# Kernel optimization log

Measured on AMD Instinct MI355X. Metric: run time of the kernel, lower is better.

Reference implementation:

```python
import jax, jax.numpy as jnp
import numpy as np

N_HEADS = 2

def setup_inputs() -> dict:
    key = jax.random.key(0)
    ks = jax.random.split(key, 10)
    d, bank, b, t = 192, 1000, 16, 4096
    s = 1.0 / np.sqrt(d)
    return {
        "z": jax.random.normal(ks[0], (b, d, t), jnp.float32),
        "memory_bank": jax.random.normal(ks[1], (d, bank), jnp.float32),
        "Wq": jax.random.normal(ks[2], (d, d), jnp.float32) * s,
        "bq": jax.random.normal(ks[3], (d,), jnp.float32) * 0.02,
        "Wk": jax.random.normal(ks[4], (d, d), jnp.float32) * s,
        "bk": jax.random.normal(ks[5], (d,), jnp.float32) * 0.02,
        "Wv": jax.random.normal(ks[6], (d, d), jnp.float32) * s,
        "bv": jax.random.normal(ks[7], (d,), jnp.float32) * 0.02,
        "Wo": jax.random.normal(ks[8], (d, d), jnp.float32) * s,
        "bo": jax.random.normal(ks[9], (d,), jnp.float32) * 0.02,
    }


def _split_heads(x):
    # x: [b, d, t] -> [b, h, t, dk]  (matches view(b, h, dk, t).transpose(2, 3))
    b, d, t = x.shape
    dk = d // N_HEADS
    return x.reshape(b, N_HEADS, dk, t).transpose(0, 1, 3, 2)


def reference(z, memory_bank, Wq, bq, Wk, bk, Wv, bv, Wo, bo):
    b, d, t = z.shape
    dk = d // N_HEADS
    # memory bank expanded over batch: [b, d, bank]
    c = jnp.broadcast_to(memory_bank[None], (b,) + memory_bank.shape)
    # 1x1 conv projections == per-channel linear
    q = jnp.einsum('oc,bct->bot', Wq, z) + bq[None, :, None]
    k = jnp.einsum('oc,bcs->bos', Wk, c) + bk[None, :, None]
    v = jnp.einsum('oc,bcs->bos', Wv, c) + bv[None, :, None]
    qh = _split_heads(q)  # [b, h, t, dk]
    kh = _split_heads(k)  # [b, h, bank, dk]
    vh = _split_heads(v)  # [b, h, bank, dk]
    scores = jnp.einsum('bhtd,bhsd->bhts', qh, kh) / jnp.sqrt(jnp.asarray(dk, z.dtype))
    p = jax.nn.softmax(scores, axis=-1)  # [b, h, t, bank]
    out = jnp.einsum('bhts,bhsd->bhtd', p, vh)  # [b, h, t, dk]
    out = out.transpose(0, 1, 3, 2).reshape(b, d, t)  # merge heads -> [b, d, t]
    return jnp.einsum('oc,bct->bot', Wo, out) + bo[None, :, None]
```

## Files before the change

### kernel.cpp

```cpp
#include <hip/hip_runtime.h>


typedef float  f32x4  __attribute__((ext_vector_type(4)));
typedef __bf16 bf16;
typedef __bf16 bf16x8 __attribute__((ext_vector_type(8)));

#define B_   16
#define D_   192
#define T_   4096
#define BANK 1000
#define SP   1024
#define DK   96
#define SCALE 0.10206207261596577f
#define LOG2E 1.4426950408889634f

__global__ __launch_bounds__(256) void pre_kernel(
    const float* __restrict__ z, bf16* __restrict__ zT,
    const float* __restrict__ mb,
    const float* __restrict__ Wk, const float* __restrict__ bk,
    const float* __restrict__ Wv, const float* __restrict__ bv,
    bf16* __restrict__ ktg, bf16* __restrict__ vtg) {
  __shared__ __align__(16) bf16 sT[64 * 200];
  const int tid = threadIdx.x;
  if (blockIdx.y < 16) {
    const int t0 = blockIdx.x * 64, b = blockIdx.y;
#pragma unroll
    for (int it = 0; it < 48; ++it) {
      int e = tid + 256 * it;
      int c = e >> 6, tl = e & 63;
      sT[tl * 200 + c] = (bf16)z[((size_t)b * D_ + c) * T_ + t0 + tl];
    }
    __syncthreads();
#pragma unroll
    for (int it = 0; it < 6; ++it) {
      int g = tid + 256 * it;
      int tl = g / 24, c8 = (g % 24) * 8;
      bf16x8 v = *(const bf16x8*)&sT[tl * 200 + c8];
      *(bf16x8*)&zT[((size_t)b * T_ + t0 + tl) * D_ + c8] = v;
    }
  } else {
    int idx = (blockIdx.y - 16) * 64 + blockIdx.x;
    int s = (idx & 3) * 256 + tid;
    int o = idx >> 2;
    int h = o / DK, i = o % DK;
    float ak = 0.f, av = 0.f;
    if (s < BANK) {
      ak = bk[o]; av = bv[o];
      for (int c = 0; c < D_; ++c) {
        float m = mb[c * BANK + s];
        ak += Wk[o * D_ + c] * m;
        av += Wv[o * D_ + c] * m;
      }
    }
    ktg[(size_t)(h * SP + s) * DK + i] = (bf16)ak;
    vtg[(size_t)(h * DK + i) * SP + s] = (bf16)av;
  }
}

template <typename OT>
__global__ __launch_bounds__(256) void proj_kernel(
    const bf16* __restrict__ XT, const float* __restrict__ W,
    const float* __restrict__ bias, OT* __restrict__ Y, float outscale) {
  __shared__ __align__(16) char smem[40960];
  bf16* sA = (bf16*)smem;
  bf16* sB = (bf16*)(smem + 16384);
  float* sE = (float*)smem;

  const int tid = threadIdx.x;
  const int t0 = blockIdx.x * 256, o0 = blockIdx.y * 64, b = blockIdx.z;
  const int lane = tid & 63, wv = tid >> 6;
  const int quad = lane >> 4, l15 = lane & 15;

  const bf16* ap[4];
#pragma unroll
  for (int r = 0; r < 4; ++r) {
    int g = tid + 256 * r;
    int tg = g >> 6, qd = (g >> 4) & 3, l5 = g & 15;
    ap[r] = &XT[((size_t)b * T_ + t0 + tg * 16 + l5) * D_ + qd * 8];
  }
  bf16x8 areg[4];
#pragma unroll
  for (int r = 0; r < 4; ++r) areg[r] = *(const bf16x8*)ap[r];

#pragma unroll
  for (int r = 0; r < 6; ++r) {
    int g = tid + 256 * r;
    int kb = g >> 8, nt = (g >> 6) & 3, qd = (g >> 4) & 3, l5 = g & 15;
    const float* wp = &W[(o0 + nt * 16 + l5) * D_ + kb * 32 + qd * 8];
    f32x4 wa = *(const f32x4*)wp, wb = *(const f32x4*)(wp + 4);
    bf16x8 pk;
#pragma unroll
    for (int u = 0; u < 4; ++u) { pk[u] = (bf16)wa[u]; pk[4 + u] = (bf16)wb[u]; }
    *(bf16x8*)&sB[(size_t)g * 8] = pk;
  }

  f32x4 acc[4][4];
#pragma unroll
  for (int m = 0; m < 4; ++m)
#pragma unroll
    for (int n = 0; n < 4; ++n) acc[m][n] = (f32x4){0.f, 0.f, 0.f, 0.f};

  for (int kb = 0; kb < 6; ++kb) {
    __syncthreads();
#pragma unroll
    for (int r = 0; r < 4; ++r)
      *(bf16x8*)&sA[(size_t)(tid + 256 * r) * 8] = areg[r];
    __syncthreads();
    if (kb < 5) {
#pragma unroll
      for (int r = 0; r < 4; ++r)
        areg[r] = *(const bf16x8*)(ap[r] + (kb + 1) * 32);
    }
    bf16x8 bf[4];
#pragma unroll
    for (int n = 0; n < 4; ++n)
      bf[n] = *(const bf16x8*)&sB[(size_t)((kb * 4 + n) * 64 + lane) * 8];
#pragma unroll
    for (int m = 0; m < 4; ++m) {
      bf16x8 af = *(const bf16x8*)&sA[(size_t)((wv * 4 + m) * 64 + lane) * 8];
#pragma unroll
      for (int n = 0; n < 4; ++n)
        acc[m][n] = __builtin_amdgcn_mfma_f32_16x16x32_bf16(af, bf[n], acc[m][n], 0, 0, 0);
    }
  }
  __syncthreads();

  float bs[4];
#pragma unroll
  for (int n = 0; n < 4; ++n) bs[n] = bias[o0 + n * 16 + l15];
  float* se = sE + wv * 1088;
#pragma unroll
  for (int m = 0; m < 4; ++m) {
#pragma unroll
    for (int n = 0; n < 4; ++n)
#pragma unroll
      for (int r = 0; r < 4; ++r)
        se[(quad * 4 + r) * 68 + n * 16 + l15] = (acc[m][n][r] + bs[n]) * outscale;
#pragma unroll
    for (int oo = 0; oo < 16; ++oo) {
      int ol = oo * 4 + quad;
      Y[((size_t)b * D_ + o0 + ol) * T_ + t0 + wv * 64 + m * 16 + l15] =
          (OT)se[l15 * 68 + ol];
    }
  }
}

__global__ __launch_bounds__(512) void attn_kernel(
    const bf16* __restrict__ qws, const bf16* __restrict__ ktg,
    const bf16* __restrict__ vtg, bf16* __restrict__ owsT) {
  __shared__ __align__(16) char smem[32768];
  bf16* kt = (bf16*)smem;
  bf16* vt = (bf16*)(smem + 12288);
  bf16* sP = (bf16*)(smem + 24576);
  bf16* qt = (bf16*)smem;

  const int tid = threadIdx.x;
  const int t0 = blockIdx.x * 128, h = blockIdx.y, b = blockIdx.z;
  const int lane = tid & 63, wv = tid >> 6;
  const int quad = lane >> 4, l15 = lane & 15;

  const bf16* kb_g = ktg + (size_t)h * SP * DK;
  const bf16* vb_g = vtg + (size_t)h * DK * SP;

  const bf16* sp_ptr[3];
  int sp_str[3];
#pragma unroll
  for (int r = 0; r < 3; ++r) {
    int g = tid + 512 * r;
    if (g < 768) {
      int kb = g >> 8, n = (g >> 6) & 3, qd = (g >> 4) & 3, l5 = g & 15;
      sp_ptr[r] = kb_g + (size_t)(n * 16 + l5) * DK + kb * 32 + qd * 8;
      sp_str[r] = 64 * DK;
    } else {
      int gv = g - 768, blk = gv >> 6;
      int kbv = blk / 6, n = blk % 6, qd = (gv >> 4) & 3, l5 = gv & 15;
      sp_ptr[r] = vb_g + (size_t)(n * 16 + l5) * SP + kbv * 32 + qd * 8;
      sp_str[r] = 64;
    }
  }
  bf16x8 kreg[3];
#pragma unroll
  for (int r = 0; r < 3; ++r) kreg[r] = *(const bf16x8*)sp_ptr[r];

#pragma unroll
  for (int r = 0; r < 3; ++r) {
    int g8 = tid + 512 * r;
    int i = g8 >> 4, t8 = (g8 & 15) * 8;
    bf16x8 v = *(const bf16x8*)&qws[((size_t)(b * D_ + h * DK + i)) * T_ + t0 + t8];
    int kb = i >> 5, qd = (i >> 3) & 3, j = i & 7;
#pragma unroll
    for (int tt = 0; tt < 8; ++tt) {
      int t = t8 + tt;
      int G = (kb * 8 + (t >> 4)) * 64 + qd * 16 + (t & 15);
      int Gs = G ^ ((G >> 6) & 7);
      qt[(size_t)Gs * 8 + j] = v[tt];
    }
  }
  __syncthreads();
  bf16x8 qf[3];
#pragma unroll
  for (int kb = 0; kb < 3; ++kb) {
    int G = (kb * 8 + wv) * 64 + lane;
    int Gs = G ^ ((G >> 6) & 7);
    qf[kb] = *(const bf16x8*)&qt[(size_t)Gs * 8];
  }

  f32x4 oacc[6];
#pragma unroll
  for (int n = 0; n < 6; ++n) oacc[n] = (f32x4){0.f, 0.f, 0.f, 0.f};
  float m_run[4] = {-1e30f, -1e30f, -1e30f, -1e30f};
  float l_run[4] = {0.f, 0.f, 0.f, 0.f};

  for (int ch = 0; ch < 16; ++ch) {
    __syncthreads();
#pragma unroll
    for (int r = 0; r < 3; ++r)
      *(bf16x8*)(smem + (size_t)(tid + 512 * r) * 16) = kreg[r];
    __syncthreads();
    if (ch < 15) {
#pragma unroll
      for (int r = 0; r < 3; ++r) {
        sp_ptr[r] += sp_str[r];
        kreg[r] = *(const bf16x8*)sp_ptr[r];
      }
    }

    f32x4 sacc[4];
#pragma unroll
    for (int n = 0; n < 4; ++n) sacc[n] = (f32x4){0.f, 0.f, 0.f, 0.f};
#pragma unroll
    for (int kb = 0; kb < 3; ++kb) {
#pragma unroll
      for (int n = 0; n < 4; ++n) {
        bf16x8 bfm = *(const bf16x8*)&kt[(size_t)((kb * 4 + n) * 64 + lane) * 8];
        sacc[n] = __builtin_amdgcn_mfma_f32_16x16x32_bf16(qf[kb], bfm, sacc[n], 0, 0, 0);
      }
    }
    if (ch == 15) {
#pragma unroll
      for (int r = 0; r < 4; ++r) {
        if (l15 >= 8) sacc[2][r] = -1e30f;
        sacc[3][r] = -1e30f;
      }
    }

    float mc[4];
#pragma unroll
    for (int r = 0; r < 4; ++r) {
      float m0 = fmaxf(fmaxf(sacc[0][r], sacc[1][r]), fmaxf(sacc[2][r], sacc[3][r]));
      m0 = fmaxf(m0, __shfl_xor(m0, 1, 64));
      m0 = fmaxf(m0, __shfl_xor(m0, 2, 64));
      m0 = fmaxf(m0, __shfl_xor(m0, 4, 64));
      m0 = fmaxf(m0, __shfl_xor(m0, 8, 64));
      mc[r] = m0;
    }
    bool keep = (mc[0] - m_run[0] <= 8.f) && (mc[1] - m_run[1] <= 8.f) &&
                (mc[2] - m_run[2] <= 8.f) && (mc[3] - m_run[3] <= 8.f);
    if (!__all(keep)) {
#pragma unroll
      for (int r = 0; r < 4; ++r) {
        float mn = fmaxf(m_run[r], mc[r]);
        float al = exp2f(m_run[r] - mn);
        m_run[r] = mn;
        l_run[r] *= al;
#pragma unroll
        for (int n = 0; n < 6; ++n) oacc[n][r] *= al;
      }
    }
    float pr[4][4];
#pragma unroll
    for (int r = 0; r < 4; ++r) {
      float ls = 0.f;
#pragma unroll
      for (int n = 0; n < 4; ++n) { pr[n][r] = exp2f(sacc[n][r] - m_run[r]); ls += pr[n][r]; }
      ls += __shfl_xor(ls, 1, 64);
      ls += __shfl_xor(ls, 2, 64);
      ls += __shfl_xor(ls, 4, 64);
      ls += __shfl_xor(ls, 8, 64);
      l_run[r] += ls;
    }

#pragma unroll
    for (int kb = 0; kb < 2; ++kb) {
#pragma unroll
      for (int nn = 0; nn < 2; ++nn) {
        int n = kb * 2 + nn;
        int qd2 = (nn << 1) | (l15 >> 3), j = l15 & 7;
#pragma unroll
        for (int r = 0; r < 4; ++r) {
          int g0 = qd2 * 16 + quad * 4 + r;
          int gs = g0 ^ ((g0 >> 3) & 7);
          sP[(size_t)(wv * 64 + gs) * 8 + j] = (bf16)pr[n][r];
        }
      }
      int gl = lane ^ ((lane >> 3) & 7);
      bf16x8 pa = *(const bf16x8*)&sP[(size_t)(wv * 64 + gl) * 8];
#pragma unroll
      for (int n2 = 0; n2 < 6; ++n2) {
        bf16x8 vf = *(const bf16x8*)&vt[(size_t)((kb * 6 + n2) * 64 + lane) * 8];
        oacc[n2] = __builtin_amdgcn_mfma_f32_16x16x32_bf16(pa, vf, oacc[n2], 0, 0, 0);
      }
    }
  }

  float inv[4];
#pragma unroll
  for (int r = 0; r < 4; ++r) inv[r] = 1.0f / l_run[r];
  __syncthreads();
  bf16* sOw = (bf16*)smem + wv * (96 * 17);
#pragma unroll
  for (int n2 = 0; n2 < 6; ++n2)
#pragma unroll
    for (int r = 0; r < 4; ++r)
      sOw[(n2 * 16 + l15) * 17 + quad * 4 + r] = (bf16)(oacc[n2][r] * inv[r]);
#pragma unroll
  for (int r2 = 0; r2 < 24; ++r2) {
    int g = r2 * 64 + lane;
    int tl = g / 96, i = g % 96;
    owsT[((size_t)b * T_ + t0 + wv * 16 + tl) * D_ + h * DK + i] = sOw[i * 17 + tl];
  }
}

extern "C" void kernel_launch(void* const* d_in, const int* in_sizes, int n_in,
                              void* d_out, int out_size, void* d_ws, size_t ws_size,
                              hipStream_t stream) {
  const float* z  = (const float*)d_in[0];
  const float* mb = (const float*)d_in[1];
  const float* Wq = (const float*)d_in[2];
  const float* bq = (const float*)d_in[3];
  const float* Wk = (const float*)d_in[4];
  const float* bk = (const float*)d_in[5];
  const float* Wv = (const float*)d_in[6];
  const float* bv = (const float*)d_in[7];
  const float* Wo = (const float*)d_in[8];
  const float* bo = (const float*)d_in[9];
  float* out = (float*)d_out;

  bf16* ktg  = (bf16*)d_ws;
  bf16* vtg  = ktg + 2 * SP * DK;
  bf16* zT   = vtg + 2 * DK * SP;
  bf16* owsT = zT + (size_t)B_ * T_ * D_;
  bf16* qws  = owsT + (size_t)B_ * T_ * D_;

  pre_kernel        <<<dim3(64, 28),          256, 0, stream>>>(z, zT, mb, Wk, bk, Wv, bv,
                                                                ktg, vtg);
  proj_kernel<bf16> <<<dim3(T_ / 256, 3, B_), 256, 0, stream>>>(zT, Wq, bq, qws,
                                                                SCALE * LOG2E);
  attn_kernel       <<<dim3(T_ / 128, 2, B_), 512, 0, stream>>>(qws, ktg, vtg, owsT);
  proj_kernel<float><<<dim3(T_ / 256, 3, B_), 256, 0, stream>>>(owsT, Wo, bo, out, 1.0f);
}
```

Measured before the change: 282.8 us.

## Fuse Q projection into attention kernel and compute row sums via MFMA

Removes the separate Q projection launch and its bf16 Q workspace round trip. Each attention block now computes its own Q tile from zT and Wq with MFMA, converting Wq to bf16 on the fly, then applies bias and scale before staging Q in shared memory. The softmax row-sum is also accumulated with an extra MFMA against a ones vector instead of shuffle reductions. The cost is extra per-block work and global reads of Wq, repeated across the 16 batch blocks, plus an added MFMA in the inner loop.

```diff
diff --git a/kernel.cpp b/kernel.cpp
--- a/kernel.cpp
+++ b/kernel.cpp
@@ -146,22 +146,64 @@
 }
 
 __global__ __launch_bounds__(512) void attn_kernel(
-    const bf16* __restrict__ qws, const bf16* __restrict__ ktg,
+    const bf16* __restrict__ zT, const float* __restrict__ Wq,
+    const float* __restrict__ bq, const bf16* __restrict__ ktg,
     const bf16* __restrict__ vtg, bf16* __restrict__ owsT) {
   __shared__ __align__(16) char smem[32768];
   bf16* kt = (bf16*)smem;
   bf16* vt = (bf16*)(smem + 12288);
   bf16* sP = (bf16*)(smem + 24576);
   bf16* qt = (bf16*)smem;
+  bf16* PA = (bf16*)smem;
+  bf16* PB = (bf16*)(smem + 8192);
 
   const int tid = threadIdx.x;
   const int t0 = blockIdx.x * 128, h = blockIdx.y, b = blockIdx.z;
   const int lane = tid & 63, wv = tid >> 6;
   const int quad = lane >> 4, l15 = lane & 15;
 
+  const bf16* qa_p;
+  {
+    int tg = tid >> 6, qd = (tid >> 4) & 3, l5 = tid & 15;
+    qa_p = &zT[((size_t)b * T_ + t0 + tg * 16 + l5) * D_ + qd * 8];
+  }
+  const float* wq_p =
+      &Wq[(size_t)(h * DK + ((tid >> 6) & 7) * 16 + (tid & 15)) * D_ + ((tid >> 4) & 3) * 8];
+  bf16x8 qa_r = *(const bf16x8*)qa_p;
+  f32x4 wqa = (f32x4){0.f, 0.f, 0.f, 0.f}, wqb = (f32x4){0.f, 0.f, 0.f, 0.f};
+  if (tid < 384) { wqa = *(const f32x4*)wq_p; wqb = *(const f32x4*)(wq_p + 4); }
+
+  f32x4 qacc[6];
+#pragma unroll
+  for (int n = 0; n < 6; ++n) qacc[n] = (f32x4){0.f, 0.f, 0.f, 0.f};
+
+  for (int kb = 0; kb < 6; ++kb) {
+    __syncthreads();
+    *(bf16x8*)&PA[(size_t)tid * 8] = qa_r;
+    if (tid < 384) {
+      bf16x8 pk;
+#pragma unroll
+      for (int u = 0; u < 4; ++u) { pk[u] = (bf16)wqa[u]; pk[4 + u] = (bf16)wqb[u]; }
+      *(bf16x8*)&PB[(size_t)tid * 8] = pk;
+    }
+    __syncthreads();
+    if (kb < 5) {
+      qa_r = *(const bf16x8*)(qa_p + (kb + 1) * 32);
+      if (tid < 384) {
+        wqa = *(const f32x4*)(wq_p + (kb + 1) * 32);
+        wqb = *(const f32x4*)(wq_p + (kb + 1) * 32 + 4);
+      }
+    }
+    bf16x8 af = *(const bf16x8*)&PA[(size_t)(wv * 64 + lane) * 8];
+#pragma unroll
+    for (int n = 0; n < 6; ++n) {
+      bf16x8 bfr = *(const bf16x8*)&PB[(size_t)(n * 64 + lane) * 8];
+      qacc[n] = __builtin_amdgcn_mfma_f32_16x16x32_bf16(af, bfr, qacc[n], 0, 0, 0);
+    }
+  }
+
   const bf16* kb_g = ktg + (size_t)h * SP * DK;
   const bf16* vb_g = vtg + (size_t)h * DK * SP;
-
   const bf16* sp_ptr[3];
   int sp_str[3];
 #pragma unroll
@@ -182,18 +224,18 @@
 #pragma unroll
   for (int r = 0; r < 3; ++r) kreg[r] = *(const bf16x8*)sp_ptr[r];
 
-#pragma unroll
-  for (int r = 0; r < 3; ++r) {
-    int g8 = tid + 512 * r;
-    int i = g8 >> 4, t8 = (g8 & 15) * 8;
-    bf16x8 v = *(const bf16x8*)&qws[((size_t)(b * D_ + h * DK + i)) * T_ + t0 + t8];
-    int kb = i >> 5, qd = (i >> 3) & 3, j = i & 7;
-#pragma unroll
-    for (int tt = 0; tt < 8; ++tt) {
-      int t = t8 + tt;
-      int G = (kb * 8 + (t >> 4)) * 64 + qd * 16 + (t & 15);
+  __syncthreads();
+#pragma unroll
+  for (int n = 0; n < 6; ++n) {
+    float bqv = bq[h * DK + n * 16 + l15];
+#pragma unroll
+    for (int r = 0; r < 4; ++r) {
+      float val = (qacc[n][r] + bqv) * (SCALE * LOG2E);
+      int i = n * 16 + l15;
+      int kbi = i >> 5, qd = (i >> 3) & 3, j = i & 7;
+      int G = (kbi * 8 + wv) * 64 + qd * 16 + quad * 4 + r;
       int Gs = G ^ ((G >> 6) & 7);
-      qt[(size_t)Gs * 8 + j] = v[tt];
+      qt[(size_t)Gs * 8 + j] = (bf16)val;
     }
   }
   __syncthreads();
@@ -205,11 +247,15 @@
     qf[kb] = *(const bf16x8*)&qt[(size_t)Gs * 8];
   }
 
+  bf16x8 ones;
+#pragma unroll
+  for (int u = 0; u < 8; ++u) ones[u] = (bf16)1.0f;
+
   f32x4 oacc[6];
 #pragma unroll
   for (int n = 0; n < 6; ++n) oacc[n] = (f32x4){0.f, 0.f, 0.f, 0.f};
+  f32x4 lacc = (f32x4){0.f, 0.f, 0.f, 0.f};
   float m_run[4] = {-1e30f, -1e30f, -1e30f, -1e30f};
-  float l_run[4] = {0.f, 0.f, 0.f, 0.f};
 
   for (int ch = 0; ch < 16; ++ch) {
     __syncthreads();
@@ -262,23 +308,16 @@
         float mn = fmaxf(m_run[r], mc[r]);
         float al = exp2f(m_run[r] - mn);
         m_run[r] = mn;
-        l_run[r] *= al;
+        lacc[r] *= al;
 #pragma unroll
         for (int n = 0; n < 6; ++n) oacc[n][r] *= al;
       }
     }
     float pr[4][4];
 #pragma unroll
-    for (int r = 0; r < 4; ++r) {
-      float ls = 0.f;
-#pragma unroll
-      for (int n = 0; n < 4; ++n) { pr[n][r] = exp2f(sacc[n][r] - m_run[r]); ls += pr[n][r]; }
-      ls += __shfl_xor(ls, 1, 64);
-      ls += __shfl_xor(ls, 2, 64);
-      ls += __shfl_xor(ls, 4, 64);
-      ls += __shfl_xor(ls, 8, 64);
-      l_run[r] += ls;
-    }
+    for (int r = 0; r < 4; ++r)
+#pragma unroll
+      for (int n = 0; n < 4; ++n) pr[n][r] = exp2f(sacc[n][r] - m_run[r]);
 
 #pragma unroll
     for (int kb = 0; kb < 2; ++kb) {
@@ -295,6 +334,7 @@
       }
       int gl = lane ^ ((lane >> 3) & 7);
       bf16x8 pa = *(const bf16x8*)&sP[(size_t)(wv * 64 + gl) * 8];
+      lacc = __builtin_amdgcn_mfma_f32_16x16x32_bf16(pa, ones, lacc, 0, 0, 0);
 #pragma unroll
       for (int n2 = 0; n2 < 6; ++n2) {
         bf16x8 vf = *(const bf16x8*)&vt[(size_t)((kb * 6 + n2) * 64 + lane) * 8];
@@ -305,7 +345,7 @@
 
   float inv[4];
 #pragma unroll
-  for (int r = 0; r < 4; ++r) inv[r] = 1.0f / l_run[r];
+  for (int r = 0; r < 4; ++r) inv[r] = 1.0f / lacc[r];
   __syncthreads();
   bf16* sOw = (bf16*)smem + wv * (96 * 17);
 #pragma unroll
@@ -340,12 +380,9 @@
   bf16* vtg  = ktg + 2 * SP * DK;
   bf16* zT   = vtg + 2 * DK * SP;
   bf16* owsT = zT + (size_t)B_ * T_ * D_;
-  bf16* qws  = owsT + (size_t)B_ * T_ * D_;
 
   pre_kernel        <<<dim3(64, 28),          256, 0, stream>>>(z, zT, mb, Wk, bk, Wv, bv,
                                                                 ktg, vtg);
-  proj_kernel<bf16> <<<dim3(T_ / 256, 3, B_), 256, 0, stream>>>(zT, Wq, bq, qws,
-                                                                SCALE * LOG2E);
-  attn_kernel       <<<dim3(T_ / 128, 2, B_), 512, 0, stream>>>(qws, ktg, vtg, owsT);
+  attn_kernel       <<<dim3(T_ / 128, 2, B_), 512, 0, stream>>>(zT, Wq, bq, ktg, vtg, owsT);
   proj_kernel<float><<<dim3(T_ / 256, 3, B_), 256, 0, stream>>>(owsT, Wo, bo, out, 1.0f);
 }
```

Measured after the change: 253.9 us. 1.11x faster.

## Fuse Q projection into attention kernel and transpose score MFMA layout

Applied to the files above, without the earlier changes.

The separate Q-projection launch and its bf16 workspace round trip are removed. Each attention block now computes its Q tile with MFMAs straight from zT and Wq, applying bias, scale and log2e. The score and PV MFMAs are transposed so each lane owns one query row, which collapses the softmax reductions to two shuffles and lets the output be written directly as packed bf16x4 instead of going through LDS. The output projection kernel also drops its LDS staging for the A operand and keeps it in registers. In exchange, every attention block reconverts Wq from fp32 on the fly, adding redundant weight loads and register pressure.

```diff
diff --git a/kernel.cpp b/kernel.cpp
--- a/kernel.cpp
+++ b/kernel.cpp
@@ -3,6 +3,7 @@
 
 typedef float  f32x4  __attribute__((ext_vector_type(4)));
 typedef __bf16 bf16;
+typedef __bf16 bf16x4 __attribute__((ext_vector_type(4)));
 typedef __bf16 bf16x8 __attribute__((ext_vector_type(8)));
 
 #define B_   16
@@ -61,9 +62,8 @@
 __global__ __launch_bounds__(256) void proj_kernel(
     const bf16* __restrict__ XT, const float* __restrict__ W,
     const float* __restrict__ bias, OT* __restrict__ Y, float outscale) {
-  __shared__ __align__(16) char smem[40960];
-  bf16* sA = (bf16*)smem;
-  bf16* sB = (bf16*)(smem + 16384);
+  __shared__ __align__(16) char smem[24576];
+  bf16* sB = (bf16*)smem;
   float* sE = (float*)smem;
 
   const int tid = threadIdx.x;
@@ -73,14 +73,11 @@
 
   const bf16* ap[4];
 #pragma unroll
-  for (int r = 0; r < 4; ++r) {
-    int g = tid + 256 * r;
-    int tg = g >> 6, qd = (g >> 4) & 3, l5 = g & 15;
-    ap[r] = &XT[((size_t)b * T_ + t0 + tg * 16 + l5) * D_ + qd * 8];
-  }
-  bf16x8 areg[4];
-#pragma unroll
-  for (int r = 0; r < 4; ++r) areg[r] = *(const bf16x8*)ap[r];
+  for (int m = 0; m < 4; ++m)
+    ap[m] = &XT[((size_t)b * T_ + t0 + (wv * 4 + m) * 16 + l15) * D_ + quad * 8];
+  bf16x8 acur[4];
+#pragma unroll
+  for (int m = 0; m < 4; ++m) acur[m] = *(const bf16x8*)ap[m];
 
 #pragma unroll
   for (int r = 0; r < 6; ++r) {
@@ -100,27 +97,26 @@
 #pragma unroll
     for (int n = 0; n < 4; ++n) acc[m][n] = (f32x4){0.f, 0.f, 0.f, 0.f};
 
+  __syncthreads();
   for (int kb = 0; kb < 6; ++kb) {
-    __syncthreads();
-#pragma unroll
-    for (int r = 0; r < 4; ++r)
-      *(bf16x8*)&sA[(size_t)(tid + 256 * r) * 8] = areg[r];
-    __syncthreads();
+    bf16x8 anext[4];
     if (kb < 5) {
 #pragma unroll
-      for (int r = 0; r < 4; ++r)
-        areg[r] = *(const bf16x8*)(ap[r] + (kb + 1) * 32);
+      for (int m = 0; m < 4; ++m)
+        anext[m] = *(const bf16x8*)(ap[m] + (kb + 1) * 32);
     }
     bf16x8 bf[4];
 #pragma unroll
     for (int n = 0; n < 4; ++n)
       bf[n] = *(const bf16x8*)&sB[(size_t)((kb * 4 + n) * 64 + lane) * 8];
 #pragma unroll
-    for (int m = 0; m < 4; ++m) {
-      bf16x8 af = *(const bf16x8*)&sA[(size_t)((wv * 4 + m) * 64 + lane) * 8];
+    for (int m = 0; m < 4; ++m)
 #pragma unroll
       for (int n = 0; n < 4; ++n)
-        acc[m][n] = __builtin_amdgcn_mfma_f32_16x16x32_bf16(af, bf[n], acc[m][n], 0, 0, 0);
+        acc[m][n] = __builtin_amdgcn_mfma_f32_16x16x32_bf16(acur[m], bf[n], acc[m][n], 0, 0, 0);
+    if (kb < 5) {
+#pragma unroll
+      for (int m = 0; m < 4; ++m) acur[m] = anext[m];
     }
   }
   __syncthreads();
@@ -146,7 +142,8 @@
 }
 
 __global__ __launch_bounds__(512) void attn_kernel(
-    const bf16* __restrict__ qws, const bf16* __restrict__ ktg,
+    const bf16* __restrict__ zT, const float* __restrict__ Wq,
+    const float* __restrict__ bq, const bf16* __restrict__ ktg,
     const bf16* __restrict__ vtg, bf16* __restrict__ owsT) {
   __shared__ __align__(16) char smem[32768];
   bf16* kt = (bf16*)smem;
@@ -161,7 +158,6 @@
 
   const bf16* kb_g = ktg + (size_t)h * SP * DK;
   const bf16* vb_g = vtg + (size_t)h * DK * SP;
-
   const bf16* sp_ptr[3];
   int sp_str[3];
 #pragma unroll
@@ -182,34 +178,43 @@
 #pragma unroll
   for (int r = 0; r < 3; ++r) kreg[r] = *(const bf16x8*)sp_ptr[r];
 
-#pragma unroll
-  for (int r = 0; r < 3; ++r) {
-    int g8 = tid + 512 * r;
-    int i = g8 >> 4, t8 = (g8 & 15) * 8;
-    bf16x8 v = *(const bf16x8*)&qws[((size_t)(b * D_ + h * DK + i)) * T_ + t0 + t8];
-    int kb = i >> 5, qd = (i >> 3) & 3, j = i & 7;
-#pragma unroll
-    for (int tt = 0; tt < 8; ++tt) {
-      int t = t8 + tt;
-      int G = (kb * 8 + (t >> 4)) * 64 + qd * 16 + (t & 15);
-      int Gs = G ^ ((G >> 6) & 7);
-      qt[(size_t)Gs * 8 + j] = v[tt];
-    }
-  }
-  __syncthreads();
+  f32x4 qacc[6];
+#pragma unroll
+  for (int n = 0; n < 6; ++n) qacc[n] = (f32x4){0.f, 0.f, 0.f, 0.f};
+  const bf16*  zrow = &zT[((size_t)b * T_ + t0 + wv * 16 + l15) * D_ + quad * 8];
+  const float* wrow = &Wq[(size_t)(h * DK + l15) * D_ + quad * 8];
+  for (int kb = 0; kb < 6; ++kb) {
+    bf16x8 zf = *(const bf16x8*)(zrow + kb * 32);
+#pragma unroll
+    for (int n = 0; n < 6; ++n) {
+      const float* wp = wrow + (size_t)n * 16 * D_ + kb * 32;
+      f32x4 wa = *(const f32x4*)wp, wb = *(const f32x4*)(wp + 4);
+      bf16x8 wf;
+#pragma unroll
+      for (int u = 0; u < 4; ++u) { wf[u] = (bf16)wa[u]; wf[4 + u] = (bf16)wb[u]; }
+      qacc[n] = __builtin_amdgcn_mfma_f32_16x16x32_bf16(wf, zf, qacc[n], 0, 0, 0);
+    }
+  }
+#pragma unroll
+  for (int n = 0; n < 6; ++n) {
+    f32x4 bq4 = *(const f32x4*)&bq[h * DK + n * 16 + quad * 4];
+    int g = ((n & 1) * 2 + (quad >> 1)) * 16 + l15;
+    int gs = g ^ ((g >> 3) & 7);
+    bf16x4 pk;
+#pragma unroll
+    for (int r = 0; r < 4; ++r)
+      pk[r] = (bf16)((qacc[n][r] + bq4[r]) * (SCALE * LOG2E));
+    *(bf16x4*)&qt[(size_t)(((n >> 1) * 8 + wv) * 64 + gs) * 8 + (quad & 1) * 4] = pk;
+  }
   bf16x8 qf[3];
 #pragma unroll
-  for (int kb = 0; kb < 3; ++kb) {
-    int G = (kb * 8 + wv) * 64 + lane;
-    int Gs = G ^ ((G >> 6) & 7);
-    qf[kb] = *(const bf16x8*)&qt[(size_t)Gs * 8];
-  }
-
-  f32x4 oacc[6];
-#pragma unroll
-  for (int n = 0; n < 6; ++n) oacc[n] = (f32x4){0.f, 0.f, 0.f, 0.f};
-  float m_run[4] = {-1e30f, -1e30f, -1e30f, -1e30f};
-  float l_run[4] = {0.f, 0.f, 0.f, 0.f};
+  for (int kb = 0; kb < 3; ++kb)
+    qf[kb] = *(const bf16x8*)&qt[(size_t)((kb * 8 + wv) * 64 + (lane ^ ((lane >> 3) & 7))) * 8];
+
+  f32x4 oaccT[6];
+#pragma unroll
+  for (int n = 0; n < 6; ++n) oaccT[n] = (f32x4){0.f, 0.f, 0.f, 0.f};
+  float m_run = -1e30f, l_run = 0.f;
 
   for (int ch = 0; ch < 16; ++ch) {
     __syncthreads();
@@ -225,99 +230,78 @@
       }
     }
 
-    f32x4 sacc[4];
-#pragma unroll
-    for (int n = 0; n < 4; ++n) sacc[n] = (f32x4){0.f, 0.f, 0.f, 0.f};
+    f32x4 scT[4];
+#pragma unroll
+    for (int n = 0; n < 4; ++n) scT[n] = (f32x4){0.f, 0.f, 0.f, 0.f};
 #pragma unroll
     for (int kb = 0; kb < 3; ++kb) {
 #pragma unroll
       for (int n = 0; n < 4; ++n) {
-        bf16x8 bfm = *(const bf16x8*)&kt[(size_t)((kb * 4 + n) * 64 + lane) * 8];
-        sacc[n] = __builtin_amdgcn_mfma_f32_16x16x32_bf16(qf[kb], bfm, sacc[n], 0, 0, 0);
+        bf16x8 kf = *(const bf16x8*)&kt[(size_t)((kb * 4 + n) * 64 + lane) * 8];
+        scT[n] = __builtin_amdgcn_mfma_f32_16x16x32_bf16(kf, qf[kb], scT[n], 0, 0, 0);
       }
     }
     if (ch == 15) {
 #pragma unroll
       for (int r = 0; r < 4; ++r) {
-        if (l15 >= 8) sacc[2][r] = -1e30f;
-        sacc[3][r] = -1e30f;
-      }
-    }
-
-    float mc[4];
-#pragma unroll
-    for (int r = 0; r < 4; ++r) {
-      float m0 = fmaxf(fmaxf(sacc[0][r], sacc[1][r]), fmaxf(sacc[2][r], sacc[3][r]));
-      m0 = fmaxf(m0, __shfl_xor(m0, 1, 64));
-      m0 = fmaxf(m0, __shfl_xor(m0, 2, 64));
-      m0 = fmaxf(m0, __shfl_xor(m0, 4, 64));
-      m0 = fmaxf(m0, __shfl_xor(m0, 8, 64));
-      mc[r] = m0;
-    }
-    bool keep = (mc[0] - m_run[0] <= 8.f) && (mc[1] - m_run[1] <= 8.f) &&
-                (mc[2] - m_run[2] <= 8.f) && (mc[3] - m_run[3] <= 8.f);
-    if (!__all(keep)) {
-#pragma unroll
-      for (int r = 0; r < 4; ++r) {
-        float mn = fmaxf(m_run[r], mc[r]);
-        float al = exp2f(m_run[r] - mn);
-        m_run[r] = mn;
-        l_run[r] *= al;
-#pragma unroll
-        for (int n = 0; n < 6; ++n) oacc[n][r] *= al;
-      }
+        scT[3][r] = -1e30f;
+        if (quad >= 2) scT[2][r] = -1e30f;
+      }
+    }
+
+    float m0 = -1e30f;
+#pragma unroll
+    for (int n = 0; n < 4; ++n)
+#pragma unroll
+      for (int r = 0; r < 4; ++r) m0 = fmaxf(m0, scT[n][r]);
+    m0 = fmaxf(m0, __shfl_xor(m0, 16, 64));
+    m0 = fmaxf(m0, __shfl_xor(m0, 32, 64));
+    if (!__all(m0 - m_run <= 8.f)) {
+      float mn = fmaxf(m_run, m0);
+      float al = exp2f(m_run - mn);
+      m_run = mn;
+      l_run *= al;
+#pragma unroll
+      for (int n = 0; n < 6; ++n)
+#pragma unroll
+        for (int r = 0; r < 4; ++r) oaccT[n][r] *= al;
     }
     float pr[4][4];
-#pragma unroll
-    for (int r = 0; r < 4; ++r) {
-      float ls = 0.f;
-#pragma unroll
-      for (int n = 0; n < 4; ++n) { pr[n][r] = exp2f(sacc[n][r] - m_run[r]); ls += pr[n][r]; }
-      ls += __shfl_xor(ls, 1, 64);
-      ls += __shfl_xor(ls, 2, 64);
-      ls += __shfl_xor(ls, 4, 64);
-      ls += __shfl_xor(ls, 8, 64);
-      l_run[r] += ls;
-    }
-
-#pragma unroll
-    for (int kb = 0; kb < 2; ++kb) {
-#pragma unroll
-      for (int nn = 0; nn < 2; ++nn) {
-        int n = kb * 2 + nn;
-        int qd2 = (nn << 1) | (l15 >> 3), j = l15 & 7;
-#pragma unroll
-        for (int r = 0; r < 4; ++r) {
-          int g0 = qd2 * 16 + quad * 4 + r;
-          int gs = g0 ^ ((g0 >> 3) & 7);
-          sP[(size_t)(wv * 64 + gs) * 8 + j] = (bf16)pr[n][r];
-        }
-      }
-      int gl = lane ^ ((lane >> 3) & 7);
-      bf16x8 pa = *(const bf16x8*)&sP[(size_t)(wv * 64 + gl) * 8];
+    float ls = 0.f;
+#pragma unroll
+    for (int n = 0; n < 4; ++n)
+#pragma unroll
+      for (int r = 0; r < 4; ++r) { pr[n][r] = exp2f(scT[n][r] - m_run); ls += pr[n][r]; }
+    ls += __shfl_xor(ls, 16, 64);
+    ls += __shfl_xor(ls, 32, 64);
+    l_run += ls;
+
+#pragma unroll
+    for (int kb2 = 0; kb2 < 2; ++kb2) {
+#pragma unroll
+      for (int nh = 0; nh < 2; ++nh) {
+        int n = kb2 * 2 + nh;
+        int g = (nh * 2 + (quad >> 1)) * 16 + l15;
+        int gs = g ^ ((g >> 3) & 7);
+        bf16x4 pk = {(bf16)pr[n][0], (bf16)pr[n][1], (bf16)pr[n][2], (bf16)pr[n][3]};
+        *(bf16x4*)&sP[(size_t)(wv * 64 + gs) * 8 + (quad & 1) * 4] = pk;
+      }
+      bf16x8 pa = *(const bf16x8*)&sP[(size_t)(wv * 64 + (lane ^ ((lane >> 3) & 7))) * 8];
 #pragma unroll
       for (int n2 = 0; n2 < 6; ++n2) {
-        bf16x8 vf = *(const bf16x8*)&vt[(size_t)((kb * 6 + n2) * 64 + lane) * 8];
-        oacc[n2] = __builtin_amdgcn_mfma_f32_16x16x32_bf16(pa, vf, oacc[n2], 0, 0, 0);
-      }
-    }
-  }
-
-  float inv[4];
-#pragma unroll
-  for (int r = 0; r < 4; ++r) inv[r] = 1.0f / l_run[r];
-  __syncthreads();
-  bf16* sOw = (bf16*)smem + wv * (96 * 17);
-#pragma unroll
-  for (int n2 = 0; n2 < 6; ++n2)
-#pragma unroll
-    for (int r = 0; r < 4; ++r)
-      sOw[(n2 * 16 + l15) * 17 + quad * 4 + r] = (bf16)(oacc[n2][r] * inv[r]);
-#pragma unroll
-  for (int r2 = 0; r2 < 24; ++r2) {
-    int g = r2 * 64 + lane;
-    int tl = g / 96, i = g % 96;
-    owsT[((size_t)b * T_ + t0 + wv * 16 + tl) * D_ + h * DK + i] = sOw[i * 17 + tl];
+        bf16x8 vf = *(const bf16x8*)&vt[(size_t)((kb2 * 6 + n2) * 64 + lane) * 8];
+        oaccT[n2] = __builtin_amdgcn_mfma_f32_16x16x32_bf16(vf, pa, oaccT[n2], 0, 0, 0);
+      }
+    }
+  }
+
+  float inv = 1.0f / l_run;
+  bf16* orow = &owsT[((size_t)b * T_ + t0 + wv * 16 + l15) * D_ + h * DK + quad * 4];
+#pragma unroll
+  for (int n2 = 0; n2 < 6; ++n2) {
+    bf16x4 pk = {(bf16)(oaccT[n2][0] * inv), (bf16)(oaccT[n2][1] * inv),
+                 (bf16)(oaccT[n2][2] * inv), (bf16)(oaccT[n2][3] * inv)};
+    *(bf16x4*)&orow[n2 * 16] = pk;
   }
 }
 
@@ -340,12 +324,9 @@
   bf16* vtg  = ktg + 2 * SP * DK;
   bf16* zT   = vtg + 2 * DK * SP;
   bf16* owsT = zT + (size_t)B_ * T_ * D_;
-  bf16* qws  = owsT + (size_t)B_ * T_ * D_;
 
   pre_kernel        <<<dim3(64, 28),          256, 0, stream>>>(z, zT, mb, Wk, bk, Wv, bv,
                                                                 ktg, vtg);
-  proj_kernel<bf16> <<<dim3(T_ / 256, 3, B_), 256, 0, stream>>>(zT, Wq, bq, qws,
-                                                                SCALE * LOG2E);
-  attn_kernel       <<<dim3(T_ / 128, 2, B_), 512, 0, stream>>>(qws, ktg, vtg, owsT);
+  attn_kernel       <<<dim3(T_ / 128, 2, B_), 512, 0, stream>>>(zT, Wq, bq, ktg, vtg, owsT);
   proj_kernel<float><<<dim3(T_ / 256, 3, B_), 256, 0, stream>>>(owsT, Wo, bo, out, 1.0f);
 }
```

Result: faster. 268.6 us (-5.0%).
